# Performance work log

Measured on AMD Instinct MI355X. Metric: run time of the kernel, lower is better.

The kernel has to match this reference:

```python
import jax, jax.numpy as jnp
import numpy as np

CUTOFF = 3.0   # self.cutoff
RMIN = 3.5     # rmin in cutoff_function (note rmin > cutoff, faithful to source)
ETA = 4.0
N_RADIAL = 5
N_3BODY = 12
NATOMS = 2048
K = 48         # neighbors per atom (equal counts -> ragged loop becomes dense batch)
HID = 64
NPAIRS = NATOMS * K


def setup_inputs() -> dict:
    key = jax.random.key(0)
    ks = jax.random.split(key, 4)
    # displacements scaled so |rij| is mostly within a few Angstrom
    rij = jax.random.normal(ks[0], (NPAIRS, 3), jnp.float32) * 1.5
    # sorted-by-atom pair list with K neighbors per atom
    unique_i = jnp.repeat(jnp.arange(NATOMS, dtype=jnp.int64), K)
    W1 = jax.random.normal(ks[1], (N_RADIAL + N_3BODY, HID), jnp.float32) * 0.1
    b1 = jnp.zeros((HID,), jnp.float32)
    W2 = jax.random.normal(ks[2], (HID, HID), jnp.float32) * 0.1
    b2 = jnp.zeros((HID,), jnp.float32)
    W3 = jax.random.normal(ks[3], (HID, 1), jnp.float32) * 0.1
    b3 = jnp.zeros((1,), jnp.float32)
    return dict(rij=rij, unique_i=unique_i, W1=W1, b1=b1, W2=W2, b2=b2, W3=W3, b3=b3)


def _energy(rij, W1, b1, W2, b2, W3, b3):
    d = jnp.linalg.norm(rij, axis=1, keepdims=True)           # (P,1)
    diff_norm = rij / jnp.maximum(d, 1e-12)                   # F.normalize
    # pair cutoff (rmin=3.5, c=3.0 as in source)
    fc = jnp.where(d > RMIN,
                   0.5 + 0.5 * jnp.cos(jnp.pi * (d - RMIN) / (CUTOFF - RMIN)),
                   1.0)
    # radial Bessel basis, n = 1..5
    ns = jnp.arange(1, N_RADIAL + 1, dtype=rij.dtype)
    rbf = jnp.sqrt(2.0 / CUTOFF) * jnp.sin(ns * jnp.pi / CUTOFF * d) / d * fc  # (P,5)
    # 3-body Gaussian descriptors
    fcrik = (0.5 + 0.5 * jnp.cos(jnp.pi * d / CUTOFF))[:, 0]  # (P,)
    dn = diff_norm.reshape(NATOMS, K, 3)
    cosang = jnp.einsum('nkd,nld->nkl', dn, dn)               # (N,K,K) pairwise mm
    cosang = jnp.where(jnp.eye(K, dtype=bool)[None], 0.0, cosang)  # fill_diagonal_(0)
    mu = jnp.linspace(-1.0, 1.0, N_3BODY).astype(rij.dtype)
    w = fcrik.reshape(NATOMS, 1, K, 1)                        # fcrik broadcast on axis being summed
    g3b = jnp.sum(jnp.exp(-ETA * (cosang[..., None] - mu) ** 2) * w, axis=2)  # (N,K,12)
    g3b = g3b.reshape(NPAIRS, N_3BODY)
    desc = jnp.concatenate([rbf, g3b], axis=1)                # (P,17)
    h = jnp.tanh(desc @ W1 + b1)
    h = jnp.tanh(h @ W2 + b2)
    eij = h @ W3 + b3                                         # (P,1)
    return jnp.sum(eij * fc)


def reference(rij, unique_i, W1, b1, W2, b2, W3, b3):
    # Module output: gradients of total energy w.r.t. rij (written into beta)
    return jax.grad(_energy)(rij, W1, b1, W2, b2, W3, b3)
```

## Files before the change

### kernel.cpp

```cpp
#include <hip/hip_runtime.h>
#include <hip/hip_bf16.h>

#define NATOMS 2048
#define K 48
#define P (NATOMS * K)
#define NR 5
#define NM 12
#define ND 17
#define HID 64

#define PI_F 3.14159265358979f
#define CUT 3.0f
#define RMIN_F 3.5f
#define AFC (-6.28318530717959f)
#define POC (PI_F / CUT)
#define SQ 0.816496580927726f
#define E1C 1.45454545454545f
#define CMC (-0.132231404958678f)

__device__ unsigned short g_w1t[64 * 32];
__device__ unsigned short g_w2t[64 * 64];
__device__ unsigned short g_w2r[64 * 64];
__device__ unsigned short g_w1r[32 * 64];

using frag_ab = __attribute__((ext_vector_type(8))) short;
using frag_cd = __attribute__((ext_vector_type(4))) float;
using f2 = __attribute__((ext_vector_type(2))) float;

__device__ __forceinline__ float fast_tanh(float x) {
    const float t = __expf(2.0f * x);
    return 1.0f - 2.0f / (t + 1.0f);
}

__device__ __forceinline__ unsigned short f2bs(float x) {
    __hip_bfloat16 b = __float2bfloat16(x);
    return __builtin_bit_cast(unsigned short, b);
}

__global__ __launch_bounds__(256) void k_prep(const float* __restrict__ W1,
                                              const float* __restrict__ W2) {
    const int i = blockIdx.x * 256 + threadIdx.x;
    if (i < 2048) {
        const int n = i >> 5, k = i & 31;
        g_w1t[i] = (k < ND) ? f2bs(W1[k * HID + n]) : (unsigned short)0;
    } else if (i < 2048 + 4096) {
        const int j = i - 2048, n = j >> 6, k = j & 63;
        g_w2t[j] = f2bs(W2[k * HID + n]);
    } else if (i < 2048 + 8192) {
        const int j = i - (2048 + 4096);
        g_w2r[j] = f2bs(W2[j]);
    } else if (i < 2048 + 8192 + 2048) {
        const int j = i - (2048 + 8192), n = j >> 6;
        g_w1r[j] = (n < ND) ? f2bs(W1[j]) : (unsigned short)0;
    }
}

#define SC_OFF    0
#define H1_OFF    9408
#define GZ2_OFF   16320
#define DESC_OFF  23232
#define SGD_OFF   27072
#define SU_OFF    30720
#define SFC_OFF   31296
#define SFK_OFF   31488
#define SD_OFF    31680
#define SCM_OFF   31872
#define SM_BYTES  31920
#define SPART_OFF 9408
#define SGM_OFF   9408
#define SGU4_OFF  14016
#define ST_OFF    16320
#define SGF4_OFF  25536
#define SE_OFF    23232

__global__ __launch_bounds__(256, 5) void k_fused(const float* __restrict__ rij,
                                                  const float* __restrict__ b1,
                                                  const float* __restrict__ b2,
                                                  const float* __restrict__ W3,
                                                  const float* __restrict__ b3,
                                                  float* __restrict__ out) {
    __shared__ __align__(16) char smem[SM_BYTES];
    float* sc    = (float*)(smem + SC_OFF);
    short* h1S   = (short*)(smem + H1_OFF);
    short* gz2S  = (short*)(smem + GZ2_OFF);
    short* descS = (short*)(smem + DESC_OFF);
    float* spart = (float*)(smem + SPART_OFF);
    float* sgm   = (float*)(smem + SGM_OFF);
    float* sT    = (float*)(smem + ST_OFF);
    float* sgd   = (float*)(smem + SGD_OFF);
    float* su    = (float*)(smem + SU_OFF);
    float* sfc   = (float*)(smem + SFC_OFF);
    float* sfk   = (float*)(smem + SFK_OFF);
    float* sd    = (float*)(smem + SD_OFF);
    float* scm   = (float*)(smem + SCM_OFF);
    float* se    = (float*)(smem + SE_OFF);
    float* sgf4  = (float*)(smem + SGF4_OFF);
    float* sgu4  = (float*)(smem + SGU4_OFF);

    const int t = threadIdx.x;
    const int base3 = blockIdx.x * (K * 3);

    if (t < K) {
        const float x = rij[base3 + 3 * t];
        const float y = rij[base3 + 3 * t + 1];
        const float z = rij[base3 + 3 * t + 2];
        const float d = sqrtf(x * x + y * y + z * z);
        const float inv = 1.0f / fmaxf(d, 1e-12f);
        su[3 * t] = x * inv; su[3 * t + 1] = y * inv; su[3 * t + 2] = z * inv;
        sd[t] = d;
        sfk[t] = 0.5f + 0.5f * __cosf(POC * d);
        sfc[t] = (d > RMIN_F) ? (0.5f + 0.5f * __cosf(AFC * (d - RMIN_F))) : 1.0f;
#pragma unroll
        for (int c = ND; c < 32; c++) descS[t * 40 + c] = 0;
    }
    if (t >= 64 && t < 64 + NM) {
        const int m = t - 64;
        scm[m] = __expf(CMC * (float)(m * m));
    }
    __syncthreads();

    if (t < 192) {
        const int ch = t / 48, k = t - ch * 48;
        const float ukx = su[3 * k], uky = su[3 * k + 1], ukz = su[3 * k + 2];
        float* scrow = &sc[k * 49 + ch * 12];
        const float* sul = &su[3 * (ch * 12)];
        f2 partv[6];
#pragma unroll
        for (int i = 0; i < 6; i++) partv[i] = (f2){0.0f, 0.0f};
#pragma unroll
        for (int li = 0; li < 12; li++) {
            const int l = ch * 12 + li;
            float c = ukx * sul[3 * li] + uky * sul[3 * li + 1] + ukz * sul[3 * li + 2];
            if (k == l) c = 0.0f;
            scrow[li] = c;
            const float cp1 = c + 1.0f;
            const float e0 = __expf(-4.0f * cp1 * cp1) * sfk[l];
            const float e1 = __expf(E1C * cp1);
            const float e2s = e1 * e1;
            const f2 e2v = {e2s, e2s};
            f2 tm = {e0, e0 * e1};
            partv[0] += tm;
#pragma unroll
            for (int i = 1; i < 6; i++) { tm *= e2v; partv[i] += tm; }
        }
        float* sp = &spart[(ch * 48 + k) * 13];
#pragma unroll
        for (int i = 0; i < 6; i++) { sp[2 * i] = partv[i].x; sp[2 * i + 1] = partv[i].y; }
    } else {
#pragma unroll
        for (int r = 0; r < 4; r++) {
            const int idx = (t - 192) + 64 * r;
            if (idx < K * NR) {
                const int p = idx / NR, n = idx - NR * p;
                const float d = sd[p];
                const float s = SQ * sfc[p] / d;
                descS[p * 40 + n] = (short)f2bs(s * __sinf((float)(n + 1) * POC * d));
            }
        }
    }
    __syncthreads();

    if (t < 192) {
        const int k = t >> 2, q = t & 3;
#pragma unroll
        for (int i = 0; i < 3; i++) {
            const int m = q * 3 + i;
            const float s = spart[(0 * 48 + k) * 13 + m] + spart[(1 * 48 + k) * 13 + m]
                          + spart[(2 * 48 + k) * 13 + m] + spart[(3 * 48 + k) * 13 + m];
            descS[k * 40 + NR + m] = (short)f2bs(s * scm[m]);
        }
    }
    __syncthreads();

    const int w = t >> 6, lane = t & 63, quad = lane >> 4, lm = lane & 15;
    const int n0 = w * 16 + lm;

    float t1[3][4];
    {
        const frag_ab bf = *(const frag_ab*)&g_w1t[n0 * 32 + quad * 8];
        const float bias = b1[n0];
#pragma unroll
        for (int mt = 0; mt < 3; mt++) {
            const frag_ab a = *(const frag_ab*)&descS[(mt * 16 + lm) * 40 + quad * 8];
            frag_cd acc = {bias, bias, bias, bias};
            acc = __builtin_amdgcn_mfma_f32_16x16x32_bf16(a, bf, acc, 0, 0, 0);
#pragma unroll
            for (int r = 0; r < 4; r++) {
                const float tv = fast_tanh(acc[r]);
                t1[mt][r] = tv;
                h1S[(mt * 16 + quad * 4 + r) * 72 + n0] = (short)f2bs(tv);
            }
        }
    }
    __syncthreads();

    {
        const frag_ab b0 = *(const frag_ab*)&g_w2t[n0 * 64 + quad * 8];
        const frag_ab b1f = *(const frag_ab*)&g_w2t[n0 * 64 + 32 + quad * 8];
        const float bias = b2[n0];
        const float w3n = W3[n0];
#pragma unroll
        for (int mt = 0; mt < 3; mt++) {
            const frag_ab a0 = *(const frag_ab*)&h1S[(mt * 16 + lm) * 72 + quad * 8];
            const frag_ab a1 = *(const frag_ab*)&h1S[(mt * 16 + lm) * 72 + 32 + quad * 8];
            frag_cd acc = {bias, bias, bias, bias};
            acc = __builtin_amdgcn_mfma_f32_16x16x32_bf16(a0, b0, acc, 0, 0, 0);
            acc = __builtin_amdgcn_mfma_f32_16x16x32_bf16(a1, b1f, acc, 0, 0, 0);
            float ep[4];
#pragma unroll
            for (int r = 0; r < 4; r++) {
                const int row = mt * 16 + quad * 4 + r;
                const float tv = fast_tanh(acc[r]);
                ep[r] = tv * w3n;
                gz2S[row * 72 + n0] = (short)f2bs(sfc[row] * w3n * (1.0f - tv * tv));
            }
#pragma unroll
            for (int off = 1; off < 16; off <<= 1) {
#pragma unroll
                for (int r = 0; r < 4; r++) ep[r] += __shfl_xor(ep[r], off, 64);
            }
            if (lm == 0) {
#pragma unroll
                for (int r = 0; r < 4; r++) se[w * 48 + mt * 16 + quad * 4 + r] = ep[r];
            }
        }
    }
    __syncthreads();

    {
        const frag_ab b0 = *(const frag_ab*)&g_w2r[n0 * 64 + quad * 8];
        const frag_ab b1f = *(const frag_ab*)&g_w2r[n0 * 64 + 32 + quad * 8];
#pragma unroll
        for (int mt = 0; mt < 3; mt++) {
            const frag_ab a0 = *(const frag_ab*)&gz2S[(mt * 16 + lm) * 72 + quad * 8];
            const frag_ab a1 = *(const frag_ab*)&gz2S[(mt * 16 + lm) * 72 + 32 + quad * 8];
            frag_cd acc = {0.0f, 0.0f, 0.0f, 0.0f};
            acc = __builtin_amdgcn_mfma_f32_16x16x32_bf16(a0, b0, acc, 0, 0, 0);
            acc = __builtin_amdgcn_mfma_f32_16x16x32_bf16(a1, b1f, acc, 0, 0, 0);
#pragma unroll
            for (int r = 0; r < 4; r++) {
                const float g = acc[r] * (1.0f - t1[mt][r] * t1[mt][r]);
                h1S[(mt * 16 + quad * 4 + r) * 72 + n0] = (short)f2bs(g);
            }
        }
    }
    __syncthreads();

    for (int tid = w; tid < 6; tid += 4) {
        const int mt = tid >> 1, nt = tid & 1, n = nt * 16 + lm;
        const frag_ab b0 = *(const frag_ab*)&g_w1r[n * 64 + quad * 8];
        const frag_ab b1f = *(const frag_ab*)&g_w1r[n * 64 + 32 + quad * 8];
        const frag_ab a0 = *(const frag_ab*)&h1S[(mt * 16 + lm) * 72 + quad * 8];
        const frag_ab a1 = *(const frag_ab*)&h1S[(mt * 16 + lm) * 72 + 32 + quad * 8];
        frag_cd acc = {0.0f, 0.0f, 0.0f, 0.0f};
        acc = __builtin_amdgcn_mfma_f32_16x16x32_bf16(a0, b0, acc, 0, 0, 0);
        acc = __builtin_amdgcn_mfma_f32_16x16x32_bf16(a1, b1f, acc, 0, 0, 0);
        if (n < ND) {
#pragma unroll
            for (int r = 0; r < 4; r++)
                sgd[(mt * 16 + quad * 4 + r) * 19 + n] = acc[r];
        }
    }
    if (t < K)
        sgd[t * 19 + 17] = se[t] + se[48 + t] + se[96 + t] + se[144 + t] + b3[0];
    __syncthreads();

    if (t < 192) {
        const int k = t >> 2, q = t & 3;
#pragma unroll
        for (int i = 0; i < 3; i++) {
            const int m = q * 3 + i;
            const float g = sgd[k * 19 + NR + m] * scm[m];
            *(f2*)&sgm[k * 24 + 2 * m] = (f2){g, (float)m * g};
        }
    }
    __syncthreads();

    if (t < 192) {
        const int ch = t / 48, k = t - ch * 48;
        f2 gm[NM];
#pragma unroll
        for (int m = 0; m < NM; m++) gm[m] = *(const f2*)&sgm[k * 24 + 2 * m];
        float* scrow = &sc[k * 49 + ch * 12];
        float* strow = &sT[k * 48 + ch * 12];
#pragma unroll
        for (int li = 0; li < 12; li++) {
            const int l = ch * 12 + li;
            const float cp1 = scrow[li] + 1.0f;
            const float e0 = __expf(-4.0f * cp1 * cp1);
            const float x = __expf(E1C * cp1);
            const f2 xx = {x, x};
            f2 pd = gm[11];
#pragma unroll
            for (int m = 10; m >= 1; m--) pd = __builtin_elementwise_fma(pd, xx, gm[m]);
            const float Pv = fmaf(pd.x, x, gm[0].x);
            const float T = e0 * Pv;
            const float U = e0 * x * pd.y;
            const float Sp = fmaf(cp1, T, -(2.0f / 11.0f) * U);
            strow[li] = T;
            scrow[li] = (k == l) ? 0.0f : (-8.0f) * Sp;
        }
    }
    __syncthreads();

    if (lane < K) {
        float s = 0.0f;
#pragma unroll
        for (int kk = 12 * w; kk < 12 * w + 12; kk++) s += sT[kk * 48 + lane];
        sgf4[w * 48 + lane] = s;

        const int k = lane;
        const float fk = sfk[k];
        float gx = 0.0f, gy = 0.0f, gz = 0.0f;
#pragma unroll
        for (int l = 12 * w; l < 12 * w + 12; l++) {
            const float wgt = fmaf(sc[k * 49 + l], sfk[l], sc[l * 49 + k] * fk);
            gx = fmaf(wgt, su[3 * l], gx);
            gy = fmaf(wgt, su[3 * l + 1], gy);
            gz = fmaf(wgt, su[3 * l + 2], gz);
        }
        sgu4[(w * 48 + k) * 3 + 0] = gx;
        sgu4[(w * 48 + k) * 3 + 1] = gy;
        sgu4[(w * 48 + k) * 3 + 2] = gz;
    }
    __syncthreads();

    if (t < K) {
        const float sgf_t = sgf4[t] + sgf4[48 + t] + sgf4[96 + t] + sgf4[144 + t];
        float gux = 0.0f, guy = 0.0f, guz = 0.0f;
#pragma unroll
        for (int ww = 0; ww < 4; ww++) {
            gux += sgu4[(ww * 48 + t) * 3 + 0];
            guy += sgu4[(ww * 48 + t) * 3 + 1];
            guz += sgu4[(ww * 48 + t) * 3 + 2];
        }
        const float d = sd[t];
        const float ux = su[3 * t], uy = su[3 * t + 1], uz = su[3 * t + 2];
        const float invd = 1.0f / d;
        float gfc = sgd[t * 19 + 17];
        float gdR = 0.0f;
#pragma unroll
        for (int n = 0; n < NR; n++) {
            const float bn = (float)(n + 1) * POC;
            float sn, cn;
            __sincosf(bn * d, &sn, &cn);
            const float g = sgd[t * 19 + n];
            gfc = fmaf(g, SQ * sn * invd, gfc);
            gdR = fmaf(g, SQ * (bn * cn - sn * invd) * invd, gdR);
        }
        const float fc = sfc[t];
        float dfc = 0.0f;
        if (d > RMIN_F) dfc = -0.5f * AFC * __sinf(AFC * (d - RMIN_F));
        const float dfcrik = -0.5f * POC * __sinf(POC * d);

        const float gd = fc * gdR + gfc * dfc + sgf_t * dfcrik;
        const float dot = gux * ux + guy * uy + guz * uz;

        out[base3 + 3 * t + 0] = fmaf(gd, ux, (gux - dot * ux) * invd);
        out[base3 + 3 * t + 1] = fmaf(gd, uy, (guy - dot * uy) * invd);
        out[base3 + 3 * t + 2] = fmaf(gd, uz, (guz - dot * uz) * invd);
    }
}

extern "C" void kernel_launch(void* const* d_in, const int* in_sizes, int n_in,
                              void* d_out, int out_size, void* d_ws, size_t ws_size,
                              hipStream_t stream) {
    (void)in_sizes; (void)n_in; (void)out_size; (void)d_ws; (void)ws_size;
    const float* rij = (const float*)d_in[0];
    const float* W1 = (const float*)d_in[2];
    const float* b1 = (const float*)d_in[3];
    const float* W2 = (const float*)d_in[4];
    const float* b2 = (const float*)d_in[5];
    const float* W3 = (const float*)d_in[6];
    const float* b3 = (const float*)d_in[7];
    float* out = (float*)d_out;

    k_prep<<<48, 256, 0, stream>>>(W1, W2);
    k_fused<<<NATOMS, 256, 0, stream>>>(rij, b1, b2, W3, b3, out);
}
```

Before: 95.86 us.

## Use native exp2/rcp/rsq intrinsics, pack unit vectors with distance, drop a barrier stage

Replaces __expf and division with the hardware exp2, rcp and rsq intrinsics using pre-scaled log2 constants. Packs each pair's unit vector and distance into one float4 in shared memory so vector LDS loads can be used. Folds the scm scaling into the MFMA gradient store, which removes a separate staging pass and one __syncthreads. Pads the sT row stride to 49 to avoid bank conflicts. The approximate rcp and rsq intrinsics may slightly change numerical precision.

```diff
diff --git a/kernel.cpp b/kernel.cpp
--- a/kernel.cpp
+++ b/kernel.cpp
@@ -17,6 +17,9 @@
 #define SQ 0.816496580927726f
 #define E1C 1.45454545454545f
 #define CMC (-0.132231404958678f)
+#define N4L (-5.77078016355585f)
+#define E1L (2.09846551402031f)
+#define TL2 (2.88539008177793f)
 
 __device__ unsigned short g_w1t[64 * 32];
 __device__ unsigned short g_w2t[64 * 64];
@@ -26,10 +29,11 @@
 using frag_ab = __attribute__((ext_vector_type(8))) short;
 using frag_cd = __attribute__((ext_vector_type(4))) float;
 using f2 = __attribute__((ext_vector_type(2))) float;
+using f4 = __attribute__((ext_vector_type(4))) float;
 
 __device__ __forceinline__ float fast_tanh(float x) {
-    const float t = __expf(2.0f * x);
-    return 1.0f - 2.0f / (t + 1.0f);
+    const float t = __builtin_amdgcn_exp2f(TL2 * x);
+    return 1.0f - 2.0f * __builtin_amdgcn_rcpf(t + 1.0f);
 }
 
 __device__ __forceinline__ unsigned short f2bs(float x) {
@@ -61,16 +65,14 @@
 #define DESC_OFF  23232
 #define SGD_OFF   27072
 #define SU_OFF    30720
-#define SFC_OFF   31296
-#define SFK_OFF   31488
-#define SD_OFF    31680
+#define SFC_OFF   31488
+#define SFK_OFF   31680
 #define SCM_OFF   31872
 #define SM_BYTES  31920
 #define SPART_OFF 9408
-#define SGM_OFF   9408
+#define ST_OFF    16320
+#define SGF4_OFF  25728
 #define SGU4_OFF  14016
-#define ST_OFF    16320
-#define SGF4_OFF  25536
 #define SE_OFF    23232
 
 __global__ __launch_bounds__(256, 5) void k_fused(const float* __restrict__ rij,
@@ -85,13 +87,11 @@
     short* gz2S  = (short*)(smem + GZ2_OFF);
     short* descS = (short*)(smem + DESC_OFF);
     float* spart = (float*)(smem + SPART_OFF);
-    float* sgm   = (float*)(smem + SGM_OFF);
     float* sT    = (float*)(smem + ST_OFF);
     float* sgd   = (float*)(smem + SGD_OFF);
     float* su    = (float*)(smem + SU_OFF);
     float* sfc   = (float*)(smem + SFC_OFF);
     float* sfk   = (float*)(smem + SFK_OFF);
-    float* sd    = (float*)(smem + SD_OFF);
     float* scm   = (float*)(smem + SCM_OFF);
     float* se    = (float*)(smem + SE_OFF);
     float* sgf4  = (float*)(smem + SGF4_OFF);
@@ -104,10 +104,10 @@
         const float x = rij[base3 + 3 * t];
         const float y = rij[base3 + 3 * t + 1];
         const float z = rij[base3 + 3 * t + 2];
-        const float d = sqrtf(x * x + y * y + z * z);
-        const float inv = 1.0f / fmaxf(d, 1e-12f);
-        su[3 * t] = x * inv; su[3 * t + 1] = y * inv; su[3 * t + 2] = z * inv;
-        sd[t] = d;
+        float s2 = fmaxf(x * x + y * y + z * z, 1e-24f);
+        const float inv = __builtin_amdgcn_rsqf(s2);
+        const float d = s2 * inv;
+        *(f4*)&su[4 * t] = (f4){x * inv, y * inv, z * inv, d};
         sfk[t] = 0.5f + 0.5f * __cosf(POC * d);
         sfc[t] = (d > RMIN_F) ? (0.5f + 0.5f * __cosf(AFC * (d - RMIN_F))) : 1.0f;
 #pragma unroll
@@ -121,21 +121,22 @@
 
     if (t < 192) {
         const int ch = t / 48, k = t - ch * 48;
-        const float ukx = su[3 * k], uky = su[3 * k + 1], ukz = su[3 * k + 2];
+        const f4 uk = *(const f4*)&su[4 * k];
         float* scrow = &sc[k * 49 + ch * 12];
-        const float* sul = &su[3 * (ch * 12)];
+        const float* sul = &su[4 * (ch * 12)];
         f2 partv[6];
 #pragma unroll
         for (int i = 0; i < 6; i++) partv[i] = (f2){0.0f, 0.0f};
 #pragma unroll
         for (int li = 0; li < 12; li++) {
             const int l = ch * 12 + li;
-            float c = ukx * sul[3 * li] + uky * sul[3 * li + 1] + ukz * sul[3 * li + 2];
+            const f4 ul = *(const f4*)&sul[4 * li];
+            float c = uk.x * ul.x + uk.y * ul.y + uk.z * ul.z;
             if (k == l) c = 0.0f;
             scrow[li] = c;
             const float cp1 = c + 1.0f;
-            const float e0 = __expf(-4.0f * cp1 * cp1) * sfk[l];
-            const float e1 = __expf(E1C * cp1);
+            const float e0 = __builtin_amdgcn_exp2f(N4L * cp1 * cp1) * sfk[l];
+            const float e1 = __builtin_amdgcn_exp2f(E1L * cp1);
             const float e2s = e1 * e1;
             const f2 e2v = {e2s, e2s};
             f2 tm = {e0, e0 * e1};
@@ -152,8 +153,8 @@
             const int idx = (t - 192) + 64 * r;
             if (idx < K * NR) {
                 const int p = idx / NR, n = idx - NR * p;
-                const float d = sd[p];
-                const float s = SQ * sfc[p] / d;
+                const float d = su[4 * p + 3];
+                const float s = SQ * sfc[p] * __builtin_amdgcn_rcpf(d);
                 descS[p * 40 + n] = (short)f2bs(s * __sinf((float)(n + 1) * POC * d));
             }
         }
@@ -256,39 +257,32 @@
         acc = __builtin_amdgcn_mfma_f32_16x16x32_bf16(a0, b0, acc, 0, 0, 0);
         acc = __builtin_amdgcn_mfma_f32_16x16x32_bf16(a1, b1f, acc, 0, 0, 0);
         if (n < ND) {
+            const float cmul = (n >= NR) ? scm[n - NR] : 1.0f;
 #pragma unroll
             for (int r = 0; r < 4; r++)
-                sgd[(mt * 16 + quad * 4 + r) * 19 + n] = acc[r];
+                sgd[(mt * 16 + quad * 4 + r) * 19 + n] = acc[r] * cmul;
         }
     }
     if (t < K)
         sgd[t * 19 + 17] = se[t] + se[48 + t] + se[96 + t] + se[144 + t] + b3[0];
-    __syncthreads();
-
-    if (t < 192) {
-        const int k = t >> 2, q = t & 3;
-#pragma unroll
-        for (int i = 0; i < 3; i++) {
-            const int m = q * 3 + i;
-            const float g = sgd[k * 19 + NR + m] * scm[m];
-            *(f2*)&sgm[k * 24 + 2 * m] = (f2){g, (float)m * g};
-        }
-    }
     __syncthreads();
 
     if (t < 192) {
         const int ch = t / 48, k = t - ch * 48;
         f2 gm[NM];
 #pragma unroll
-        for (int m = 0; m < NM; m++) gm[m] = *(const f2*)&sgm[k * 24 + 2 * m];
+        for (int m = 0; m < NM; m++) {
+            const float g = sgd[k * 19 + NR + m];
+            gm[m] = (f2){g, (float)m * g};
+        }
         float* scrow = &sc[k * 49 + ch * 12];
-        float* strow = &sT[k * 48 + ch * 12];
+        float* strow = &sT[k * 49 + ch * 12];
 #pragma unroll
         for (int li = 0; li < 12; li++) {
             const int l = ch * 12 + li;
             const float cp1 = scrow[li] + 1.0f;
-            const float e0 = __expf(-4.0f * cp1 * cp1);
-            const float x = __expf(E1C * cp1);
+            const float e0 = __builtin_amdgcn_exp2f(N4L * cp1 * cp1);
+            const float x = __builtin_amdgcn_exp2f(E1L * cp1);
             const f2 xx = {x, x};
             f2 pd = gm[11];
 #pragma unroll
@@ -306,7 +300,7 @@
     if (lane < K) {
         float s = 0.0f;
 #pragma unroll
-        for (int kk = 12 * w; kk < 12 * w + 12; kk++) s += sT[kk * 48 + lane];
+        for (int kk = 12 * w; kk < 12 * w + 12; kk++) s += sT[kk * 49 + lane];
         sgf4[w * 48 + lane] = s;
 
         const int k = lane;
@@ -315,9 +309,10 @@
 #pragma unroll
         for (int l = 12 * w; l < 12 * w + 12; l++) {
             const float wgt = fmaf(sc[k * 49 + l], sfk[l], sc[l * 49 + k] * fk);
-            gx = fmaf(wgt, su[3 * l], gx);
-            gy = fmaf(wgt, su[3 * l + 1], gy);
-            gz = fmaf(wgt, su[3 * l + 2], gz);
+            const f4 ul = *(const f4*)&su[4 * l];
+            gx = fmaf(wgt, ul.x, gx);
+            gy = fmaf(wgt, ul.y, gy);
+            gz = fmaf(wgt, ul.z, gz);
         }
         sgu4[(w * 48 + k) * 3 + 0] = gx;
         sgu4[(w * 48 + k) * 3 + 1] = gy;
@@ -334,9 +329,10 @@
             guy += sgu4[(ww * 48 + t) * 3 + 1];
             guz += sgu4[(ww * 48 + t) * 3 + 2];
         }
-        const float d = sd[t];
-        const float ux = su[3 * t], uy = su[3 * t + 1], uz = su[3 * t + 2];
-        const float invd = 1.0f / d;
+        const f4 uv = *(const f4*)&su[4 * t];
+        const float d = uv.w;
+        const float ux = uv.x, uy = uv.y, uz = uv.z;
+        const float invd = __builtin_amdgcn_rcpf(d);
         float gfc = sgd[t * 19 + 17];
         float gdR = 0.0f;
 #pragma unroll
```

Result: faster. 92.75 us (-3.2%).
